# Kernel tuning notes

Measured on AMD Instinct MI355X. Metric: run time of the kernel, lower is better.

## Reference

```python
import jax, jax.numpy as jnp
import numpy as np

B, C_IN, H, W = 4, 256, 64, 64
LATENT = 256


def conv1x1(x, w, b):
    # x: [B, Cin, H, W], w: [Cout, Cin], b: [Cout]
    return jnp.einsum('bchw,oc->bohw', x, w) + b[None, :, None, None]


def setup_inputs() -> dict:
    key = jax.random.key(0)
    ks = jax.random.split(key, 9)
    s_in = 1.0 / np.sqrt(C_IN)
    s_lat = 1.0 / np.sqrt(LATENT)
    return {
        'x': jax.random.normal(ks[0], (B, C_IN, H, W), dtype=jnp.float32),
        'Wq': jax.random.normal(ks[1], (LATENT, C_IN), dtype=jnp.float32) * s_in,
        'bq': jax.random.normal(ks[2], (LATENT,), dtype=jnp.float32) * 0.01,
        'Wk': jax.random.normal(ks[3], (LATENT, C_IN), dtype=jnp.float32) * s_in,
        'bk': jax.random.normal(ks[4], (LATENT,), dtype=jnp.float32) * 0.01,
        'Wv': jax.random.normal(ks[5], (LATENT, C_IN), dtype=jnp.float32) * s_in,
        'bv': jax.random.normal(ks[6], (LATENT,), dtype=jnp.float32) * 0.01,
        'Wo': jax.random.normal(ks[7], (C_IN, LATENT), dtype=jnp.float32) * s_lat,
        'bo': jax.random.normal(ks[8], (C_IN,), dtype=jnp.float32) * 0.01,
    }


def reference(x, Wq, bq, Wk, bk, Wv, bv, Wo, bo):
    b, _, h, w = x.shape
    n = h * w
    q = conv1x1(x, Wq, bq).reshape(b, LATENT, n)  # [B, L, N]
    k = conv1x1(x, Wk, bk).reshape(b, LATENT, n)
    v = conv1x1(x, Wv, bv).reshape(b, LATENT, n)
    scale = jnp.sqrt(jnp.asarray(LATENT, dtype=x.dtype))
    # attention[b, i, j] = sum_c q[b, c, i] * k[b, c, j]
    attn = jnp.einsum('bci,bcj->bij', q, k) / scale
    # faithful to original: softmax over dim=1 (query index i, per column j)
    attn = jax.nn.softmax(attn, axis=1)
    # res[b, c, j] = sum_i v[b, c, i] * attn[b, i, j]
    res = jnp.einsum('bci,bij->bcj', v, attn).reshape(b, LATENT, h, w)
    return conv1x1(res, Wo, bo)
```

## Files before the change

kernel.cpp:

```cpp
#include <hip/hip_runtime.h>

#define B_  4
#define C_  256
#define N_  4096
#define SCALE 0.0625f

typedef short s8v __attribute__((ext_vector_type(8)));
typedef float f4v __attribute__((ext_vector_type(4)));

static __device__ __forceinline__ ushort f2bf(float f) {
  union { float f; uint u; } v; v.f = f;
  return (ushort)((v.u + 0x7FFFu + ((v.u >> 16) & 1u)) >> 16);
}

__global__ __launch_bounds__(256) void xpose_cast(
    const float* __restrict__ x, ushort* __restrict__ x_t)
{
  const int b  = blockIdx.z;
  const int c0 = blockIdx.y * 64;
  const int n0 = blockIdx.x * 64;
  __shared__ float t[64][65];

  const int tc = threadIdx.x >> 4;
  const int tn = (threadIdx.x & 15) * 4;
  #pragma unroll
  for (int cc = 0; cc < 64; cc += 16) {
    float4 v = *(const float4*)(x + (size_t)(b * C_ + c0 + cc + tc) * N_ + n0 + tn);
    t[cc + tc][tn + 0] = v.x;
    t[cc + tc][tn + 1] = v.y;
    t[cc + tc][tn + 2] = v.z;
    t[cc + tc][tn + 3] = v.w;
  }
  __syncthreads();

  const int on = threadIdx.x >> 2;
  const int oc = (threadIdx.x & 3) * 16;
  union { ushort us[16]; uint4 q[2]; } o;
  #pragma unroll
  for (int i = 0; i < 16; ++i) o.us[i] = f2bf(t[oc + i][on]);
  ushort* dst = x_t + (size_t)(b * N_ + n0 + on) * C_ + c0 + oc;
  *(uint4*)dst       = o.q[0];
  *(uint4*)(dst + 8) = o.q[1];
}

__global__ __launch_bounds__(256, 2) void qkv_mfma(
    const ushort* __restrict__ x_t,
    const float* __restrict__ Wq, const float* __restrict__ bq,
    const float* __restrict__ Wk, const float* __restrict__ bk,
    const float* __restrict__ Wv, const float* __restrict__ bv,
    ushort* __restrict__ q_t, ushort* __restrict__ k_t, ushort* __restrict__ v_bf)
{
  const int p = blockIdx.z >> 2;
  const int b = blockIdx.z & 3;
  const float* W  = (p == 0) ? Wq : (p == 1) ? Wk : Wv;
  const float* bi = (p == 0) ? bq : (p == 1) ? bk : bv;
  const int l0    = blockIdx.y * 64;
  const int nseg  = blockIdx.x * 512;

  const int tid  = threadIdx.x;
  const int lane = tid & 63;
  const int wave = tid >> 6;
  const int l16  = lane & 15;
  const int quad = lane >> 4;

  __shared__ __align__(16) ushort w_lds[64 * 264];
  __shared__ __align__(16) ushort x_lds[64 * 264];

  for (int g = tid; g < 4096; g += 256) {
    int row = g >> 6, col4 = (g & 63) * 4;
    float4 wv = *(const float4*)(W + (size_t)(l0 + row) * 256 + col4);
    *(ushort4*)&w_lds[row * 264 + col4] =
        make_ushort4(f2bf(wv.x), f2bf(wv.y), f2bf(wv.z), f2bf(wv.w));
  }
  __syncthreads();

  s8v kw[4][8];
  #pragma unroll
  for (int lt = 0; lt < 4; ++lt)
    #pragma unroll
    for (int cs = 0; cs < 8; ++cs)
      kw[lt][cs] = *(const s8v*)&w_lds[(lt * 16 + l16) * 264 + quad * 8 + cs * 32];

  float bias_l[4];
  #pragma unroll
  for (int lt = 0; lt < 4; ++lt) bias_l[lt] = bi[l0 + lt * 16 + l16];

  for (int it = 0; it < 8; ++it) {
    const int n0 = nseg + it * 64;
    {
      const ushort* xseg = x_t + (size_t)(b * N_ + n0) * C_;
      #pragma unroll
      for (int k = 0; k < 8; ++k) {
        int c = tid + k * 256;
        uint4 d = *(const uint4*)(xseg + (size_t)c * 8);
        *(uint4*)&x_lds[(c >> 5) * 264 + (c & 31) * 8] = d;
      }
    }
    __syncthreads();

    f4v s[4];
    #pragma unroll
    for (int lt = 0; lt < 4; ++lt) s[lt] = (f4v){0.f, 0.f, 0.f, 0.f};
    const ushort* xa_base = x_lds + (wave * 16 + l16) * 264 + quad * 8;
    #pragma unroll
    for (int cs = 0; cs < 8; ++cs) {
      s8v xa = *(const s8v*)(xa_base + cs * 32);
      #pragma unroll
      for (int lt = 0; lt < 4; ++lt)
        s[lt] = __builtin_amdgcn_mfma_f32_16x16x32_bf16(xa, kw[lt][cs], s[lt], 0, 0, 0);
    }

    const int nb = n0 + wave * 16 + quad * 4;
    if (p < 2) {
      ushort* outp = (p == 0) ? q_t : k_t;
      #pragma unroll
      for (int lt = 0; lt < 4; ++lt) {
        const int l = l0 + lt * 16 + l16;
        #pragma unroll
        for (int r = 0; r < 4; ++r)
          outp[(size_t)(b * N_ + nb + r) * C_ + l] = f2bf(s[lt][r] + bias_l[lt]);
      }
    } else {
      #pragma unroll
      for (int lt = 0; lt < 4; ++lt) {
        const int c_out = l0 + lt * 16 + l16;
        *(ushort4*)&v_bf[(size_t)(b * C_ + c_out) * N_ + nb] =
            make_ushort4(f2bf(s[lt][0] + bias_l[lt]), f2bf(s[lt][1] + bias_l[lt]),
                         f2bf(s[lt][2] + bias_l[lt]), f2bf(s[lt][3] + bias_l[lt]));
      }
    }
    __syncthreads();
  }
}

__global__ __launch_bounds__(512, 2) void flash7(
    const ushort* __restrict__ q_t, const ushort* __restrict__ k_t,
    const ushort* __restrict__ v_bf, ushort* __restrict__ res0,
    ushort* __restrict__ res1, float* __restrict__ den)
{
  const int tid  = threadIdx.x;
  const int lane = tid & 63;
  const int wave = tid >> 6;
  const int l16  = lane & 15;
  const int quad = lane >> 4;
  const int jw    = blockIdx.x * 128;
  const int seg   = blockIdx.y;
  const int ibase = seg * 2048;
  const int b     = blockIdx.z;

  const int wqk_j = wave & 3;
  const int wqk_i = wave >> 2;
  const int wpv_c = wave & 3;
  const int wpv_j = wave >> 2;

  __shared__ __align__(16) ushort q_lds[64 * 264];
  __shared__ __align__(16) ushort p_lds[128 * 72];

  s8v kf[2][8];
  #pragma unroll
  for (int jt = 0; jt < 2; ++jt) {
    const ushort* kp = k_t + (size_t)(b * N_ + jw + wqk_j * 32 + jt * 16 + l16) * C_ + quad * 8;
    #pragma unroll
    for (int cs = 0; cs < 8; ++cs) kf[jt][cs] = *(const s8v*)(kp + cs * 32);
  }

  f4v acc[4][4];
  #pragma unroll
  for (int m = 0; m < 4; ++m)
    #pragma unroll
    for (int t = 0; t < 4; ++t) acc[m][t] = (f4v){0.f, 0.f, 0.f, 0.f};
  float dacc0 = 0.f, dacc1 = 0.f;

  const ushort* vbase0 = v_bf + (size_t)(b * C_ + wpv_c * 64 + l16) * N_ + quad * 8;

  for (int it = 0; it < 32; ++it) {
    const int i0 = ibase + it * 64;

    {
      const ushort* qseg = q_t + ((size_t)(b * N_) + i0) * C_;
      int c0 = tid, c1 = tid + 512, c2 = tid + 1024, c3 = tid + 1536;
      uint4 d0 = *(const uint4*)(qseg + (size_t)c0 * 8);
      uint4 d1 = *(const uint4*)(qseg + (size_t)c1 * 8);
      uint4 d2 = *(const uint4*)(qseg + (size_t)c2 * 8);
      uint4 d3 = *(const uint4*)(qseg + (size_t)c3 * 8);
      *(uint4*)&q_lds[(c0 >> 5) * 264 + (c0 & 31) * 8] = d0;
      *(uint4*)&q_lds[(c1 >> 5) * 264 + (c1 & 31) * 8] = d1;
      *(uint4*)&q_lds[(c2 >> 5) * 264 + (c2 & 31) * 8] = d2;
      *(uint4*)&q_lds[(c3 >> 5) * 264 + (c3 & 31) * 8] = d3;
    }

    s8v av[4][2];
    #pragma unroll
    for (int m = 0; m < 4; ++m)
      #pragma unroll
      for (int ks = 0; ks < 2; ++ks)
        av[m][ks] = *(const s8v*)(vbase0 + (size_t)(m * 16) * N_ + i0 + ks * 32);

    __syncthreads();

    #pragma unroll
    for (int itile = 0; itile < 2; ++itile) {
      const int i_loc = (wqk_i * 2 + itile) * 16;
      f4v s0 = (f4v){0.f, 0.f, 0.f, 0.f};
      f4v s1 = (f4v){0.f, 0.f, 0.f, 0.f};
      const ushort* qa_base = q_lds + (i_loc + l16) * 264 + quad * 8;
      #pragma unroll
      for (int cs = 0; cs < 8; ++cs) {
        s8v qa = *(const s8v*)(qa_base + cs * 32);
        s0 = __builtin_amdgcn_mfma_f32_16x16x32_bf16(qa, kf[0][cs], s0, 0, 0, 0);
        s1 = __builtin_amdgcn_mfma_f32_16x16x32_bf16(qa, kf[1][cs], s1, 0, 0, 0);
      }
      {
        float e0 = __expf(s0[0] * SCALE), e1 = __expf(s0[1] * SCALE);
        float e2 = __expf(s0[2] * SCALE), e3 = __expf(s0[3] * SCALE);
        dacc0 += (e0 + e1) + (e2 + e3);
        *(ushort4*)&p_lds[(wqk_j * 32 + l16) * 72 + i_loc + quad * 4] =
            make_ushort4(f2bf(e0), f2bf(e1), f2bf(e2), f2bf(e3));
      }
      {
        float e0 = __expf(s1[0] * SCALE), e1 = __expf(s1[1] * SCALE);
        float e2 = __expf(s1[2] * SCALE), e3 = __expf(s1[3] * SCALE);
        dacc1 += (e0 + e1) + (e2 + e3);
        *(ushort4*)&p_lds[(wqk_j * 32 + 16 + l16) * 72 + i_loc + quad * 4] =
            make_ushort4(f2bf(e0), f2bf(e1), f2bf(e2), f2bf(e3));
      }
    }

    __syncthreads();

    #pragma unroll
    for (int ks = 0; ks < 2; ++ks) {
      s8v pb[4];
      #pragma unroll
      for (int t = 0; t < 4; ++t)
        pb[t] = *(const s8v*)&p_lds[(wpv_j * 64 + t * 16 + l16) * 72 + ks * 32 + quad * 8];
      #pragma unroll
      for (int m = 0; m < 4; ++m)
        #pragma unroll
        for (int t = 0; t < 4; ++t)
          acc[m][t] = __builtin_amdgcn_mfma_f32_16x16x32_bf16(av[m][ks], pb[t], acc[m][t], 0, 0, 0);
    }
  }

  dacc0 += __shfl_xor(dacc0, 16);  dacc0 += __shfl_xor(dacc0, 32);
  dacc1 += __shfl_xor(dacc1, 16);  dacc1 += __shfl_xor(dacc1, 32);
  if (lane < 16) {
    atomicAdd(&den[b * N_ + jw + wqk_j * 32 + lane], dacc0);
    atomicAdd(&den[b * N_ + jw + wqk_j * 32 + 16 + lane], dacc1);
  }

  ushort* rp = (seg ? res1 : res0) + (size_t)(b * N_ + jw) * C_;
  #pragma unroll
  for (int half = 0; half < 2; ++half) {
    __syncthreads();
    if (wpv_j == half) {
      #pragma unroll
      for (int m = 0; m < 4; ++m) {
        const int c0 = wpv_c * 64 + m * 16 + quad * 4;
        #pragma unroll
        for (int t = 0; t < 4; ++t) {
          const int j_loc = t * 16 + l16;
          *(ushort4*)&q_lds[j_loc * 264 + c0] =
              make_ushort4(f2bf(acc[m][t][0]), f2bf(acc[m][t][1]),
                           f2bf(acc[m][t][2]), f2bf(acc[m][t][3]));
        }
      }
    }
    __syncthreads();
    {
      const int jbase = half * 64;
      #pragma unroll
      for (int k = 0; k < 4; ++k) {
        int c = tid + k * 512;
        int row = c >> 5, col = (c & 31) * 8;
        uint4 d = *(const uint4*)&q_lds[row * 264 + col];
        *(uint4*)&rp[(size_t)(jbase + row) * C_ + col] = d;
      }
    }
  }
}

__global__ __launch_bounds__(256, 2) void out_mfma(
    const ushort* __restrict__ res0, const ushort* __restrict__ res1,
    const float* __restrict__ Wo, const float* __restrict__ bo,
    const float* __restrict__ den, float* __restrict__ out)
{
  const int b    = blockIdx.z;
  const int co0  = blockIdx.y * 64;
  const int nseg = blockIdx.x * 256;

  const int tid  = threadIdx.x;
  const int lane = tid & 63;
  const int wave = tid >> 6;
  const int l16  = lane & 15;
  const int quad = lane >> 4;

  __shared__ __align__(16) ushort w_lds[64 * 264];
  __shared__ __align__(16) ushort r_lds[2][64 * 264];

  for (int g = tid; g < 4096; g += 256) {
    int row = g >> 6, col4 = (g & 63) * 4;
    float4 wv = *(const float4*)(Wo + (size_t)(co0 + row) * 256 + col4);
    *(ushort4*)&w_lds[row * 264 + col4] =
        make_ushort4(f2bf(wv.x), f2bf(wv.y), f2bf(wv.z), f2bf(wv.w));
  }
  __syncthreads();

  s8v kw[4][8];
  #pragma unroll
  for (int lt = 0; lt < 4; ++lt)
    #pragma unroll
    for (int cs = 0; cs < 8; ++cs)
      kw[lt][cs] = *(const s8v*)&w_lds[(lt * 16 + l16) * 264 + quad * 8 + cs * 32];

  float bias_l[4];
  #pragma unroll
  for (int lt = 0; lt < 4; ++lt) bias_l[lt] = bo[co0 + lt * 16 + l16];

  for (int it = 0; it < 4; ++it) {
    const int n0 = nseg + it * 64;
    {
      const ushort* r0 = res0 + (size_t)(b * N_ + n0) * C_;
      const ushort* r1 = res1 + (size_t)(b * N_ + n0) * C_;
      #pragma unroll
      for (int k = 0; k < 8; ++k) {
        int c = tid + k * 256;
        uint4 d0 = *(const uint4*)(r0 + (size_t)c * 8);
        uint4 d1 = *(const uint4*)(r1 + (size_t)c * 8);
        *(uint4*)&r_lds[0][(c >> 5) * 264 + (c & 31) * 8] = d0;
        *(uint4*)&r_lds[1][(c >> 5) * 264 + (c & 31) * 8] = d1;
      }
    }
    __syncthreads();

    f4v s[4];
    #pragma unroll
    for (int lt = 0; lt < 4; ++lt) s[lt] = (f4v){0.f, 0.f, 0.f, 0.f};
    #pragma unroll
    for (int buf = 0; buf < 2; ++buf) {
      const ushort* ra_base = r_lds[buf] + (wave * 16 + l16) * 264 + quad * 8;
      #pragma unroll
      for (int cs = 0; cs < 8; ++cs) {
        s8v ra = *(const s8v*)(ra_base + cs * 32);
        #pragma unroll
        for (int lt = 0; lt < 4; ++lt)
          s[lt] = __builtin_amdgcn_mfma_f32_16x16x32_bf16(ra, kw[lt][cs], s[lt], 0, 0, 0);
      }
    }

    const int nb = n0 + wave * 16 + quad * 4;
    float4 dv = *(const float4*)(den + (size_t)b * N_ + nb);
    const float di0 = 1.0f / dv.x, di1 = 1.0f / dv.y, di2 = 1.0f / dv.z, di3 = 1.0f / dv.w;
    #pragma unroll
    for (int lt = 0; lt < 4; ++lt) {
      const int co = co0 + lt * 16 + l16;
      *(float4*)&out[(size_t)(b * C_ + co) * N_ + nb] =
          make_float4(s[lt][0] * di0 + bias_l[lt], s[lt][1] * di1 + bias_l[lt],
                      s[lt][2] * di2 + bias_l[lt], s[lt][3] * di3 + bias_l[lt]);
    }
    __syncthreads();
  }
}

extern "C" void kernel_launch(void* const* d_in, const int* in_sizes, int n_in,
                              void* d_out, int out_size, void* d_ws, size_t ws_size,
                              hipStream_t stream)
{
  const float* x  = (const float*)d_in[0];
  const float* Wq = (const float*)d_in[1];
  const float* bq = (const float*)d_in[2];
  const float* Wk = (const float*)d_in[3];
  const float* bk = (const float*)d_in[4];
  const float* Wv = (const float*)d_in[5];
  const float* bv = (const float*)d_in[6];
  const float* Wo = (const float*)d_in[7];
  const float* bo = (const float*)d_in[8];
  float* out = (float*)d_out;

  char* ws = (char*)d_ws;
  ushort* q_t  = (ushort*)(ws);
  ushort* k_t  = (ushort*)(ws + (size_t)8  * 1024 * 1024);
  ushort* v_bf = (ushort*)(ws + (size_t)16 * 1024 * 1024);
  ushort* res0 = (ushort*)(ws + (size_t)24 * 1024 * 1024);
  ushort* res1 = (ushort*)(ws + (size_t)32 * 1024 * 1024);
  float*  den  = (float*) (ws + (size_t)40 * 1024 * 1024);
  ushort* x_t  = (ushort*)(ws + (size_t)40 * 1024 * 1024 + 65536);

  (void)hipMemsetAsync(den, 0, (size_t)B_ * N_ * sizeof(float), stream);

  xpose_cast<<<dim3(64, 4, 4), dim3(256), 0, stream>>>(x, x_t);
  qkv_mfma <<<dim3(8, 4, 12),  dim3(256), 0, stream>>>(x_t, Wq, bq, Wk, bk, Wv, bv, q_t, k_t, v_bf);
  flash7   <<<dim3(32, 2, 4),  dim3(512), 0, stream>>>(q_t, k_t, v_bf, res0, res1, den);
  out_mfma <<<dim3(16, 4, 4),  dim3(256), 0, stream>>>(res0, res1, Wo, bo, den, out);
}
```

Before: 215.7 us.

## Halve flash attention block tile to 64 columns with 4 waves

Shrinks the attention kernel's block from 128 key columns and 8 waves to 64 columns and 4 waves, doubling the grid and raising the per-CU occupancy hint. The epilogue writes the whole result tile in one LDS staging pass instead of two halves. This gives more independent blocks to overlap barriers and latency, but each block now reloads the full Q tile for half as many columns, doubling Q traffic per unit of work.

```diff
diff --git a/kernel.cpp b/kernel.cpp
--- a/kernel.cpp
+++ b/kernel.cpp
@@ -133,7 +133,7 @@
   }
 }
 
-__global__ __launch_bounds__(512, 2) void flash7(
+__global__ __launch_bounds__(256, 3) void flash8(
     const ushort* __restrict__ q_t, const ushort* __restrict__ k_t,
     const ushort* __restrict__ v_bf, ushort* __restrict__ res0,
     ushort* __restrict__ res1, float* __restrict__ den)
@@ -143,18 +143,16 @@
   const int wave = tid >> 6;
   const int l16  = lane & 15;
   const int quad = lane >> 4;
-  const int jw    = blockIdx.x * 128;
+  const int jw    = blockIdx.x * 64;
   const int seg   = blockIdx.y;
   const int ibase = seg * 2048;
   const int b     = blockIdx.z;
 
-  const int wqk_j = wave & 3;
-  const int wqk_i = wave >> 2;
-  const int wpv_c = wave & 3;
-  const int wpv_j = wave >> 2;
+  const int wqk_j = wave & 1;
+  const int wqk_i = wave >> 1;
 
   __shared__ __align__(16) ushort q_lds[64 * 264];
-  __shared__ __align__(16) ushort p_lds[128 * 72];
+  __shared__ __align__(16) ushort p_lds[64 * 72];
 
   s8v kf[2][8];
   #pragma unroll
@@ -171,22 +169,19 @@
     for (int t = 0; t < 4; ++t) acc[m][t] = (f4v){0.f, 0.f, 0.f, 0.f};
   float dacc0 = 0.f, dacc1 = 0.f;
 
-  const ushort* vbase0 = v_bf + (size_t)(b * C_ + wpv_c * 64 + l16) * N_ + quad * 8;
+  const ushort* vbase0 = v_bf + (size_t)(b * C_ + wave * 64 + l16) * N_ + quad * 8;
 
   for (int it = 0; it < 32; ++it) {
     const int i0 = ibase + it * 64;
 
     {
       const ushort* qseg = q_t + ((size_t)(b * N_) + i0) * C_;
-      int c0 = tid, c1 = tid + 512, c2 = tid + 1024, c3 = tid + 1536;
-      uint4 d0 = *(const uint4*)(qseg + (size_t)c0 * 8);
-      uint4 d1 = *(const uint4*)(qseg + (size_t)c1 * 8);
-      uint4 d2 = *(const uint4*)(qseg + (size_t)c2 * 8);
-      uint4 d3 = *(const uint4*)(qseg + (size_t)c3 * 8);
-      *(uint4*)&q_lds[(c0 >> 5) * 264 + (c0 & 31) * 8] = d0;
-      *(uint4*)&q_lds[(c1 >> 5) * 264 + (c1 & 31) * 8] = d1;
-      *(uint4*)&q_lds[(c2 >> 5) * 264 + (c2 & 31) * 8] = d2;
-      *(uint4*)&q_lds[(c3 >> 5) * 264 + (c3 & 31) * 8] = d3;
+      #pragma unroll
+      for (int k = 0; k < 8; ++k) {
+        int c = tid + k * 256;
+        uint4 d = *(const uint4*)(qseg + (size_t)c * 8);
+        *(uint4*)&q_lds[(c >> 5) * 264 + (c & 31) * 8] = d;
+      }
     }
 
     s8v av[4][2];
@@ -233,7 +228,7 @@
       s8v pb[4];
       #pragma unroll
       for (int t = 0; t < 4; ++t)
-        pb[t] = *(const s8v*)&p_lds[(wpv_j * 64 + t * 16 + l16) * 72 + ks * 32 + quad * 8];
+        pb[t] = *(const s8v*)&p_lds[(t * 16 + l16) * 72 + ks * 32 + quad * 8];
       #pragma unroll
       for (int m = 0; m < 4; ++m)
         #pragma unroll
@@ -249,33 +244,25 @@
     atomicAdd(&den[b * N_ + jw + wqk_j * 32 + 16 + lane], dacc1);
   }
 
-  ushort* rp = (seg ? res1 : res0) + (size_t)(b * N_ + jw) * C_;
-  #pragma unroll
-  for (int half = 0; half < 2; ++half) {
-    __syncthreads();
-    if (wpv_j == half) {
-      #pragma unroll
-      for (int m = 0; m < 4; ++m) {
-        const int c0 = wpv_c * 64 + m * 16 + quad * 4;
-        #pragma unroll
-        for (int t = 0; t < 4; ++t) {
-          const int j_loc = t * 16 + l16;
-          *(ushort4*)&q_lds[j_loc * 264 + c0] =
-              make_ushort4(f2bf(acc[m][t][0]), f2bf(acc[m][t][1]),
-                           f2bf(acc[m][t][2]), f2bf(acc[m][t][3]));
-        }
-      }
-    }
-    __syncthreads();
-    {
-      const int jbase = half * 64;
-      #pragma unroll
-      for (int k = 0; k < 4; ++k) {
-        int c = tid + k * 512;
-        int row = c >> 5, col = (c & 31) * 8;
-        uint4 d = *(const uint4*)&q_lds[row * 264 + col];
-        *(uint4*)&rp[(size_t)(jbase + row) * C_ + col] = d;
-      }
+  #pragma unroll
+  for (int m = 0; m < 4; ++m) {
+    const int c0 = wave * 64 + m * 16 + quad * 4;
+    #pragma unroll
+    for (int t = 0; t < 4; ++t) {
+      *(ushort4*)&q_lds[(t * 16 + l16) * 264 + c0] =
+          make_ushort4(f2bf(acc[m][t][0]), f2bf(acc[m][t][1]),
+                       f2bf(acc[m][t][2]), f2bf(acc[m][t][3]));
+    }
+  }
+  __syncthreads();
+  {
+    ushort* rp = (seg ? res1 : res0) + (size_t)(b * N_ + jw) * C_;
+    #pragma unroll
+    for (int k = 0; k < 8; ++k) {
+      int c = tid + k * 256;
+      int row = c >> 5, col = (c & 31) * 8;
+      uint4 d = *(const uint4*)&q_lds[row * 264 + col];
+      *(uint4*)&rp[(size_t)row * C_ + col] = d;
     }
   }
 }
@@ -390,6 +377,6 @@
 
   xpose_cast<<<dim3(64, 4, 4), dim3(256), 0, stream>>>(x, x_t);
   qkv_mfma <<<dim3(8, 4, 12),  dim3(256), 0, stream>>>(x_t, Wq, bq, Wk, bk, Wv, bv, q_t, k_t, v_bf);
-  flash7   <<<dim3(32, 2, 4),  dim3(512), 0, stream>>>(q_t, k_t, v_bf, res0, res1, den);
+  flash8   <<<dim3(64, 2, 4),  dim3(256), 0, stream>>>(q_t, k_t, v_bf, res0, res1, den);
   out_mfma <<<dim3(16, 4, 4),  dim3(256), 0, stream>>>(res0, res1, Wo, bo, den, out);
 }
```

New measurement: 500.7 us. 132% more time.
